# Kernel tuning notes

Hardware: AMD Instinct MI355X
Metric: run time of the kernel (lower is better)

## Reference

```python
import jax, jax.numpy as jnp
import numpy as np

N_CLASSES = 20
N_ANCHORS = 5
OBJ_SCALE = 5.0
NOBJ_SCALE = 1.0
IOU_THRESH = 0.6  # hard-coded 0.6 in the original forward (not self.threshold)
PRIORS = [1.3221, 1.73145, 3.19275, 4.00944, 5.05587, 8.09892, 9.47112, 4.84053, 11.2364, 10.0071]


def _iou(ax, ay, aw, ah, bx, by, bw, bh):
    # IoU of center-format boxes (x, y, w, h)
    iw = jnp.maximum(jnp.minimum(ax + aw * 0.5, bx + bw * 0.5) - jnp.maximum(ax - aw * 0.5, bx - bw * 0.5), 0.0)
    ih = jnp.maximum(jnp.minimum(ay + ah * 0.5, by + bh * 0.5) - jnp.maximum(ay - ah * 0.5, by - bh * 0.5), 0.0)
    inter = iw * ih
    return inter / (aw * ah + bw * bh - inter)


def setup_inputs() -> dict:
    key = jax.random.key(0)
    k1, k2, k3 = jax.random.split(key, 3)
    B, T, H, W = 32, 50, 76, 76
    output = jax.random.normal(k1, (B, N_ANCHORS * (5 + N_CLASSES), H, W), dtype=jnp.float32)
    cls = jax.random.randint(k2, (B, T, 1), 0, N_CLASSES).astype(jnp.float32)
    boxes = jax.random.uniform(k3, (B, T, 4), dtype=jnp.float32, minval=0.02, maxval=0.98)
    target = jnp.concatenate([cls, boxes], axis=-1)  # [B, T, 5]: class, x, y, w, h
    priors = jnp.asarray(PRIORS, dtype=jnp.float32)
    return {"output": output, "target": target, "priors": priors}


def _forward(output, target, priors):
    K = 5 + N_CLASSES
    N = N_ANCHORS
    B, Z, H, W = output.shape
    T = target.shape[1]
    out = jnp.transpose(output, (0, 2, 3, 1)).reshape(B, H, W, N, K)  # [B,H,W,N,K]
    tgt = jax.lax.stop_gradient(target)               # truth is .detach()'d in the original
    pri = jax.lax.stop_gradient(priors).reshape(N, 2)
    op = jax.lax.stop_gradient(out)                   # output_postp is .detach()'d

    # decoded predicted boxes (normalized), raw outputs + grid/prior biases
    gx = jnp.arange(W, dtype=out.dtype)[None, None, :, None]
    gy = jnp.arange(H, dtype=out.dtype)[None, :, None, None]
    px = (gx + op[..., 0]) / W                        # [B,H,W,N]
    py = (gy + op[..., 1]) / H
    pw = pri[:, 0] * jnp.exp(op[..., 2]) / W
    ph = pri[:, 1] * jnp.exp(op[..., 3]) / H

    tx_, ty_, tw_, th_ = tgt[..., 1], tgt[..., 2], tgt[..., 3], tgt[..., 4]  # [B,T]

    # IoU of every predicted box vs every target -> noobj suppression mask
    ious = _iou(px[..., None], py[..., None], pw[..., None], ph[..., None],
                tx_[:, None, None, None, :], ty_[:, None, None, None, :],
                tw_[:, None, None, None, :], th_[:, None, None, None, :])  # [B,H,W,N,T]
    iou_mask = jnp.max(ious, axis=-1) > IOU_THRESH    # [B,H,W,N]

    # anchor assignment: IoU of (0,0)-shifted truth vs per-cell predicted (w,h)
    ci = jnp.floor(tx_ * W).astype(jnp.int32)         # [B,T] grid col
    cj = jnp.floor(ty_ * H).astype(jnp.int32)         # [B,T] grid row
    b_idx = jnp.arange(B, dtype=jnp.int32)[:, None]
    pw_cell = pw[b_idx, cj, ci]                       # [B,T,N]
    ph_cell = ph[b_idx, cj, ci]
    ious2 = _iou(0.0, 0.0, tw_[..., None], th_[..., None], 0.0, 0.0, pw_cell, ph_cell)  # [B,T,N]
    max_ious = jnp.max(ious2, axis=-1)                # [B,T]
    max_n = jnp.argmax(ious2, axis=-1).astype(jnp.int32)  # first max, like torch.max

    pvol = jnp.where(max_ious[..., None] != 0.0, pri[max_n], 0.0)  # [B,T,2]
    tx = tx_ * W - ci.astype(out.dtype)
    ty = ty_ * H - cj.astype(out.dtype)
    tw = jnp.log(tw_ * W / pvol[..., 0])
    th = jnp.log(th_ * H / pvol[..., 1])
    tw = jnp.where(jnp.isnan(tw), 0.0, tw)
    th = jnp.where(jnp.isnan(th), 0.0, th)
    tvol = jnp.stack([tx, ty, tw, th], axis=-1)       # [B,T,4]
    scale = 2.0 - tw_ * th_                           # [B,T] coord loss scale
    tcls = jnp.floor(tgt[..., 0]).astype(jnp.int32)   # int(cat) in one_hot_encode

    # scatter-max of flattened target id gives exactly the last duplicate.
    cell = ((b_idx * H + cj) * W + ci) * N + max_n    # [B,T] flat index into B*H*W*N
    flat_t = jnp.arange(B * T, dtype=jnp.int32).reshape(B, T)
    owner = jnp.full((B * H * W * N,), -1, dtype=jnp.int32).at[cell.reshape(-1)].max(flat_t.reshape(-1))
    pmask = (owner >= 0).reshape(B, H, W, N)          # p/o/c masks of the original
    ow = jnp.maximum(owner, 0)
    tvol_cell = tvol.reshape(B * T, 4)[ow].reshape(B, H, W, N, 4)
    scale_cell = scale.reshape(B * T)[ow].reshape(B, H, W, N)
    cls_cell = tcls.reshape(B * T)[ow].reshape(B, H, W, N)
    onehot = jax.nn.one_hot(cls_cell, N_CLASSES, dtype=out.dtype)  # [B,H,W,N,C]

    d_box = jnp.where(pmask[..., None], scale_cell[..., None] * (tvol_cell - out[..., :4]), 0.0)
    d_obj = jnp.where(pmask, OBJ_SCALE * (1.0 - out[..., 4]),
                      jnp.where(iou_mask, 0.0, NOBJ_SCALE * (0.0 - out[..., 4])))
    d_cls = jnp.where(pmask[..., None], 1.0 * (onehot - out[..., 5:]), 0.0)
    deltas = jnp.concatenate([d_box, d_obj[..., None], d_cls], axis=-1)  # [B,H,W,N,K]
    cost = jnp.sqrt(jnp.sum(deltas ** 2)) ** 2
    return cost


def reference(output, target, priors):
    return _forward(output, target, priors)
```

## Files before the change

kernel.cpp:

```cpp
#include <hip/hip_runtime.h>
#include <math.h>

#define BB 32
#define TT 50
#define HH 76
#define WW 76
#define NA 5
#define NC 20
#define KK 25
#define HW (HH*WW)
#define NMAIN 91
#define GPB 92
#define NBLK (GPB*BB)
#define THALF 25

typedef _Float16 h2 __attribute__((ext_vector_type(2)));

static __device__ __forceinline__ h2 i2h(int i) { return __builtin_bit_cast(h2, i); }
static __device__ __forceinline__ h2 f2h2(float x) {
    _Float16 h = (_Float16)x; h2 r; r.x = h; r.y = h; return r;
}
static __device__ __forceinline__ int pack2t(float x, int tid) {
    unsigned short b = __builtin_bit_cast(unsigned short, (_Float16)x);
    int lo = (int)b;
    int hi = __shfl(lo, tid + THALF, 64);
    return (lo & 0xFFFF) | (hi << 16);
}

#define IOU_STEP_PK(AX1, AX2, AY1, AY2, ACC) do {                              \
    h2 iw_ = __builtin_elementwise_min((AX2), sx2)                             \
           - __builtin_elementwise_max((AX1), sx1);                            \
    h2 ih_ = __builtin_elementwise_min((AY2), sy2)                             \
           - __builtin_elementwise_max((AY1), sy1);                            \
    iw_ = __builtin_elementwise_max(iw_, zero2);                               \
    (ACC) = __builtin_elementwise_max((ACC),                                   \
            __builtin_elementwise_fma(iw_, ih_, sna)); } while (0)

__global__ __launch_bounds__(64) void fused_kernel(
    const float* __restrict__ out, const float* __restrict__ tgt,
    const float* __restrict__ pri, float* __restrict__ partial)
{
    const int b  = blockIdx.y;
    const int gx = blockIdx.x;
    const int tid = threadIdx.x;
    const int tl = (tid < TT) ? tid : (TT - 1);
    const h2 zero2 = f2h2(0.0f);

    const float* tp = tgt + ((size_t)b * TT + tl) * 5;
    float bx = tp[1], by = tp[2], bw = tp[3], bh = tp[4];
    const int vx1i = pack2t(fmaf(-0.5f, bw, bx), tid);
    const int vx2i = pack2t(fmaf( 0.5f, bw, bx), tid);
    const int vy1i = pack2t(fmaf(-0.5f, bh, by), tid);
    const int vy2i = pack2t(fmaf( 0.5f, bh, by), tid);
    const int vnai = pack2t(-0.375f * (bw * bh), tid);

    float mysum = 0.0f;

    if (gx < NMAIN) {
        int k = gx * 64 + tid;
        float valid = (k < HW) ? 1.0f : 0.0f;
        int rem = (k < HW) ? k : (HW - 1);
        int h = rem / WW;
        int w = rem - h * WW;

        const float* op0 = out + (size_t)b * KK * NA * HW + rem;
        h2 ax1h[NA], ax2h[NA], ay1h[NA], ay2h[NA], acch[NA];
        _Float16 thr16[NA];
        float o4v[NA];
        #pragma unroll
        for (int n = 0; n < NA; ++n) {
            const float* op = op0 + (size_t)(n * KK) * HW;
            float o0 = op[0];
            float o1 = op[HW];
            float o2 = op[2*HW];
            float o3 = op[3*HW];
            o4v[n] = op[4*HW];
            float px = ((float)w + o0) * (1.0f/WW);
            float py = ((float)h + o1) * (1.0f/HH);
            float pw = pri[2*n]   * __expf(o2) * (1.0f/WW);
            float ph = pri[2*n+1] * __expf(o3) * (1.0f/HH);
            ax1h[n] = f2h2(fmaf(-0.5f, pw, px));
            ax2h[n] = f2h2(fmaf( 0.5f, pw, px));
            ay1h[n] = f2h2(fmaf(-0.5f, ph, py));
            ay2h[n] = f2h2(fmaf( 0.5f, ph, py));
            thr16[n] = (_Float16)(0.375f * (pw * ph));
            acch[n] = zero2;
        }

        #pragma unroll 5
        for (int u = 0; u < THALF; ++u) {
            h2 sx1 = i2h(__builtin_amdgcn_readlane(vx1i, u));
            h2 sx2 = i2h(__builtin_amdgcn_readlane(vx2i, u));
            h2 sy1 = i2h(__builtin_amdgcn_readlane(vy1i, u));
            h2 sy2 = i2h(__builtin_amdgcn_readlane(vy2i, u));
            h2 sna = i2h(__builtin_amdgcn_readlane(vnai, u));
            IOU_STEP_PK(ax1h[0], ax2h[0], ay1h[0], ay2h[0], acch[0]);
            IOU_STEP_PK(ax1h[1], ax2h[1], ay1h[1], ay2h[1], acch[1]);
            IOU_STEP_PK(ax1h[2], ax2h[2], ay1h[2], ay2h[2], acch[2]);
            IOU_STEP_PK(ax1h[3], ax2h[3], ay1h[3], ay2h[3], acch[3]);
            IOU_STEP_PK(ax1h[4], ax2h[4], ay1h[4], ay2h[4], acch[4]);
        }

        float s = 0.0f;
        #pragma unroll
        for (int n = 0; n < NA; ++n) {
            float m = fmaxf((float)acch[n].x, (float)acch[n].y);
            s += (m > (float)thr16[n]) ? 0.0f : o4v[n] * o4v[n];
        }
        mysum = s * valid;
    } else {
        float cls = tp[0];
        int ci = (int)floorf(bx * WW);
        int cj = (int)floorf(by * HH);

        const float* ob = out + (size_t)b * KK * NA * HW + (size_t)cj * WW + ci;
        float best = -1.0f; int bn = 0;
        #pragma unroll
        for (int n = 0; n < NA; ++n) {
            float e2 = ob[(size_t)(n*KK + 2) * HW];
            float e3 = ob[(size_t)(n*KK + 3) * HW];
            float pw = pri[2*n]   * __expf(e2) * (1.0f/WW);
            float ph = pri[2*n+1] * __expf(e3) * (1.0f/HH);
            float inter = fminf(bw, pw) * fminf(bh, ph);
            float iou = inter / (bw*bh + pw*ph - inter);
            if (iou > best) { best = iou; bn = n; }
        }
        int mycell = (cj*WW + ci)*NA + bn;

        bool dead = false;
        #pragma unroll 10
        for (int t2 = 0; t2 < TT; ++t2) {
            int c2 = __builtin_amdgcn_readlane(mycell, t2);
            dead = dead || (c2 == mycell && t2 > tid);
        }
        float live = (tid < TT && !dead) ? 1.0f : 0.0f;

        int rem = cj*WW + ci;
        const float* op = out + ((size_t)(b*NA + bn) * KK) * HW + rem;
        float o0 = op[0];
        float o1 = op[HW];
        float o2 = op[2*HW];
        float o3 = op[3*HW];
        float o4 = op[4*HW];

        float tx = bx * WW - (float)ci;
        float ty = by * HH - (float)cj;
        float tw = __logf(bw * WW / pri[2*bn]);
        float th = __logf(bh * HH / pri[2*bn+1]);
        if (tw != tw) tw = 0.0f;
        if (th != th) th = 0.0f;
        float sc = 2.0f - bw * bh;

        float d0 = sc * (tx - o0);
        float d1 = sc * (ty - o1);
        float d2 = sc * (tw - o2);
        float d3 = sc * (th - o3);
        float dob = 5.0f * (1.0f - o4);
        float s = d0*d0 + d1*d1 + d2*d2 + d3*d3 + dob*dob;
        int tc = (int)floorf(cls);
        #pragma unroll
        for (int c = 0; c < NC; ++c) {
            float oc = op[(size_t)(5 + c) * HW];
            float d = ((c == tc) ? 1.0f : 0.0f) - oc;
            s += d * d;
        }

        float px = ((float)ci + o0) * (1.0f/WW);
        float py = ((float)cj + o1) * (1.0f/HH);
        float pw = pri[2*bn]   * __expf(o2) * (1.0f/WW);
        float ph = pri[2*bn+1] * __expf(o3) * (1.0f/HH);
        h2 Ax1 = f2h2(fmaf(-0.5f, pw, px));
        h2 Ax2 = f2h2(fmaf( 0.5f, pw, px));
        h2 Ay1 = f2h2(fmaf(-0.5f, ph, py));
        h2 Ay2 = f2h2(fmaf( 0.5f, ph, py));
        _Float16 Thr16 = (_Float16)(0.375f * (pw * ph));
        h2 acc = zero2;
        #pragma unroll 5
        for (int u = 0; u < THALF; ++u) {
            h2 sx1 = i2h(__builtin_amdgcn_readlane(vx1i, u));
            h2 sx2 = i2h(__builtin_amdgcn_readlane(vx2i, u));
            h2 sy1 = i2h(__builtin_amdgcn_readlane(vy1i, u));
            h2 sy2 = i2h(__builtin_amdgcn_readlane(vy2i, u));
            h2 sna = i2h(__builtin_amdgcn_readlane(vnai, u));
            IOU_STEP_PK(Ax1, Ax2, Ay1, Ay2, acc);
        }
        float m = fmaxf((float)acc.x, (float)acc.y);
        s -= (m > (float)Thr16) ? 0.0f : o4 * o4;
        mysum = s * live;
    }

    #pragma unroll
    for (int off = 32; off > 0; off >>= 1)
        mysum += __shfl_down(mysum, off, 64);
    if (tid == 0)
        partial[b * GPB + gx] = mysum;
}

__global__ __launch_bounds__(256) void reduce_kernel(
    const float* __restrict__ partial, int n, float* __restrict__ outp)
{
    int tid = threadIdx.x;
    float s = 0.0f;
    for (int i = tid; i < n; i += 256) s += partial[i];
    #pragma unroll
    for (int off = 32; off > 0; off >>= 1)
        s += __shfl_down(s, off, 64);
    __shared__ float swave[4];
    if ((tid & 63) == 0) swave[tid >> 6] = s;
    __syncthreads();
    if (tid == 0) {
        float total = swave[0] + swave[1] + swave[2] + swave[3];
        float r = sqrtf(total);
        outp[0] = r * r;
    }
}

extern "C" void kernel_launch(void* const* d_in, const int* in_sizes, int n_in,
                              void* d_out, int out_size, void* d_ws, size_t ws_size,
                              hipStream_t stream) {
    const float* output = (const float*)d_in[0];
    const float* target = (const float*)d_in[1];
    const float* priors = (const float*)d_in[2];
    float* partial = (float*)d_ws;

    fused_kernel<<<dim3(GPB, BB), 64, 0, stream>>>(output, target, priors, partial);
    reduce_kernel<<<1, 256, 0, stream>>>(partial, NBLK, (float*)d_out);
}
```

Measured before the change: 22.59 us.

## Split target IoU loop across two wavefronts per block with LDS merge

Each block now runs two wavefronts that handle the same 64 grid cells but split the 25 packed target pairs between them (13 and 12). The second wave writes its per-anchor max accumulators to shared memory, and the first wave merges them and computes the noobj sum. This halves the serial IoU loop per wave to expose more parallelism. The cost is that both waves repeat the global loads and exp work for the cells, and a block barrier plus an LDS exchange are added. In the target blocks the second wave sits idle.

```diff
diff --git a/kernel.cpp b/kernel.cpp
--- a/kernel.cpp
+++ b/kernel.cpp
@@ -13,17 +13,19 @@
 #define GPB 92
 #define NBLK (GPB*BB)
 #define THALF 25
+#define USPLIT 13
 
 typedef _Float16 h2 __attribute__((ext_vector_type(2)));
 
 static __device__ __forceinline__ h2 i2h(int i) { return __builtin_bit_cast(h2, i); }
+static __device__ __forceinline__ int h2toi(h2 v) { return __builtin_bit_cast(int, v); }
 static __device__ __forceinline__ h2 f2h2(float x) {
     _Float16 h = (_Float16)x; h2 r; r.x = h; r.y = h; return r;
 }
-static __device__ __forceinline__ int pack2t(float x, int tid) {
+static __device__ __forceinline__ int pack2t(float x, int lane) {
     unsigned short b = __builtin_bit_cast(unsigned short, (_Float16)x);
     int lo = (int)b;
-    int hi = __shfl(lo, tid + THALF, 64);
+    int hi = __shfl(lo, lane + THALF, 64);
     return (lo & 0xFFFF) | (hi << 16);
 }
 
@@ -36,28 +38,40 @@
     (ACC) = __builtin_elementwise_max((ACC),                                   \
             __builtin_elementwise_fma(iw_, ih_, sna)); } while (0)
 
-__global__ __launch_bounds__(64) void fused_kernel(
+#define RL5(U) \
+    h2 sx1 = i2h(__builtin_amdgcn_readlane(vx1i, (U))); \
+    h2 sx2 = i2h(__builtin_amdgcn_readlane(vx2i, (U))); \
+    h2 sy1 = i2h(__builtin_amdgcn_readlane(vy1i, (U))); \
+    h2 sy2 = i2h(__builtin_amdgcn_readlane(vy2i, (U))); \
+    h2 sna = i2h(__builtin_amdgcn_readlane(vnai, (U)));
+
+__global__ __launch_bounds__(128) void fused_kernel(
     const float* __restrict__ out, const float* __restrict__ tgt,
     const float* __restrict__ pri, float* __restrict__ partial)
 {
     const int b  = blockIdx.y;
     const int gx = blockIdx.x;
-    const int tid = threadIdx.x;
-    const int tl = (tid < TT) ? tid : (TT - 1);
+    const int tid  = threadIdx.x;
+    const int wid  = tid >> 6;
+    const int lane = tid & 63;
+    const int tl = (lane < TT) ? lane : (TT - 1);
     const h2 zero2 = f2h2(0.0f);
+
+    __shared__ int   lacc[64][NA];
+    __shared__ float swave[2];
 
     const float* tp = tgt + ((size_t)b * TT + tl) * 5;
     float bx = tp[1], by = tp[2], bw = tp[3], bh = tp[4];
-    const int vx1i = pack2t(fmaf(-0.5f, bw, bx), tid);
-    const int vx2i = pack2t(fmaf( 0.5f, bw, bx), tid);
-    const int vy1i = pack2t(fmaf(-0.5f, bh, by), tid);
-    const int vy2i = pack2t(fmaf( 0.5f, bh, by), tid);
-    const int vnai = pack2t(-0.375f * (bw * bh), tid);
+    const int vx1i = pack2t(fmaf(-0.5f, bw, bx), lane);
+    const int vx2i = pack2t(fmaf( 0.5f, bw, bx), lane);
+    const int vy1i = pack2t(fmaf(-0.5f, bh, by), lane);
+    const int vy2i = pack2t(fmaf( 0.5f, bh, by), lane);
+    const int vnai = pack2t(-0.375f * (bw * bh), lane);
 
     float mysum = 0.0f;
 
     if (gx < NMAIN) {
-        int k = gx * 64 + tid;
+        int k = gx * 64 + lane;
         float valid = (k < HW) ? 1.0f : 0.0f;
         int rem = (k < HW) ? k : (HW - 1);
         int h = rem / WW;
@@ -87,28 +101,42 @@
             acch[n] = zero2;
         }
 
-        #pragma unroll 5
-        for (int u = 0; u < THALF; ++u) {
-            h2 sx1 = i2h(__builtin_amdgcn_readlane(vx1i, u));
-            h2 sx2 = i2h(__builtin_amdgcn_readlane(vx2i, u));
-            h2 sy1 = i2h(__builtin_amdgcn_readlane(vy1i, u));
-            h2 sy2 = i2h(__builtin_amdgcn_readlane(vy2i, u));
-            h2 sna = i2h(__builtin_amdgcn_readlane(vnai, u));
-            IOU_STEP_PK(ax1h[0], ax2h[0], ay1h[0], ay2h[0], acch[0]);
-            IOU_STEP_PK(ax1h[1], ax2h[1], ay1h[1], ay2h[1], acch[1]);
-            IOU_STEP_PK(ax1h[2], ax2h[2], ay1h[2], ay2h[2], acch[2]);
-            IOU_STEP_PK(ax1h[3], ax2h[3], ay1h[3], ay2h[3], acch[3]);
-            IOU_STEP_PK(ax1h[4], ax2h[4], ay1h[4], ay2h[4], acch[4]);
-        }
-
-        float s = 0.0f;
-        #pragma unroll
-        for (int n = 0; n < NA; ++n) {
-            float m = fmaxf((float)acch[n].x, (float)acch[n].y);
-            s += (m > (float)thr16[n]) ? 0.0f : o4v[n] * o4v[n];
-        }
-        mysum = s * valid;
-    } else {
+        if (wid == 0) {
+            #pragma unroll
+            for (int u = 0; u < USPLIT; ++u) {
+                RL5(u);
+                IOU_STEP_PK(ax1h[0], ax2h[0], ay1h[0], ay2h[0], acch[0]);
+                IOU_STEP_PK(ax1h[1], ax2h[1], ay1h[1], ay2h[1], acch[1]);
+                IOU_STEP_PK(ax1h[2], ax2h[2], ay1h[2], ay2h[2], acch[2]);
+                IOU_STEP_PK(ax1h[3], ax2h[3], ay1h[3], ay2h[3], acch[3]);
+                IOU_STEP_PK(ax1h[4], ax2h[4], ay1h[4], ay2h[4], acch[4]);
+            }
+        } else {
+            #pragma unroll
+            for (int u = USPLIT; u < THALF; ++u) {
+                RL5(u);
+                IOU_STEP_PK(ax1h[0], ax2h[0], ay1h[0], ay2h[0], acch[0]);
+                IOU_STEP_PK(ax1h[1], ax2h[1], ay1h[1], ay2h[1], acch[1]);
+                IOU_STEP_PK(ax1h[2], ax2h[2], ay1h[2], ay2h[2], acch[2]);
+                IOU_STEP_PK(ax1h[3], ax2h[3], ay1h[3], ay2h[3], acch[3]);
+                IOU_STEP_PK(ax1h[4], ax2h[4], ay1h[4], ay2h[4], acch[4]);
+            }
+            #pragma unroll
+            for (int n = 0; n < NA; ++n)
+                lacc[lane][n] = h2toi(acch[n]);
+        }
+        __syncthreads();
+        if (wid == 0) {
+            float s = 0.0f;
+            #pragma unroll
+            for (int n = 0; n < NA; ++n) {
+                h2 m2 = __builtin_elementwise_max(acch[n], i2h(lacc[lane][n]));
+                float m = fmaxf((float)m2.x, (float)m2.y);
+                s += (m > (float)thr16[n]) ? 0.0f : o4v[n] * o4v[n];
+            }
+            mysum = s * valid;
+        }
+    } else if (wid == 0) {
         float cls = tp[0];
         int ci = (int)floorf(bx * WW);
         int cj = (int)floorf(by * HH);
@@ -131,9 +159,9 @@
         #pragma unroll 10
         for (int t2 = 0; t2 < TT; ++t2) {
             int c2 = __builtin_amdgcn_readlane(mycell, t2);
-            dead = dead || (c2 == mycell && t2 > tid);
-        }
-        float live = (tid < TT && !dead) ? 1.0f : 0.0f;
+            dead = dead || (c2 == mycell && t2 > lane);
+        }
+        float live = (lane < TT && !dead) ? 1.0f : 0.0f;
 
         int rem = cj*WW + ci;
         const float* op = out + ((size_t)(b*NA + bn) * KK) * HW + rem;
@@ -177,11 +205,7 @@
         h2 acc = zero2;
         #pragma unroll 5
         for (int u = 0; u < THALF; ++u) {
-            h2 sx1 = i2h(__builtin_amdgcn_readlane(vx1i, u));
-            h2 sx2 = i2h(__builtin_amdgcn_readlane(vx2i, u));
-            h2 sy1 = i2h(__builtin_amdgcn_readlane(vy1i, u));
-            h2 sy2 = i2h(__builtin_amdgcn_readlane(vy2i, u));
-            h2 sna = i2h(__builtin_amdgcn_readlane(vnai, u));
+            RL5(u);
             IOU_STEP_PK(Ax1, Ax2, Ay1, Ay2, acc);
         }
         float m = fmaxf((float)acc.x, (float)acc.y);
@@ -192,8 +216,10 @@
     #pragma unroll
     for (int off = 32; off > 0; off >>= 1)
         mysum += __shfl_down(mysum, off, 64);
+    if (lane == 0) swave[wid] = mysum;
+    __syncthreads();
     if (tid == 0)
-        partial[b * GPB + gx] = mysum;
+        partial[b * GPB + gx] = swave[0] + swave[1];
 }
 
 __global__ __launch_bounds__(256) void reduce_kernel(
@@ -223,6 +249,6 @@
     const float* priors = (const float*)d_in[2];
     float* partial = (float*)d_ws;
 
-    fused_kernel<<<dim3(GPB, BB), 64, 0, stream>>>(output, target, priors, partial);
+    fused_kernel<<<dim3(GPB, BB), 128, 0, stream>>>(output, target, priors, partial);
     reduce_kernel<<<1, 256, 0, stream>>>(partial, NBLK, (float*)d_out);
 }
```

Measured after the change: 23.28 us. 3.1% more time.
